# Kernel tuning notes

Hardware: AMD Instinct MI355X
Metric: run time of the kernel (lower is better)

The kernel has to match this reference:

```python
import jax, jax.numpy as jnp
import numpy as np

B, T, D, H = 4, 2048, 1024, 16
HD = D // H  # head_size = 64
EPS = 1e-5


def layernorm(x, g, b):
    mu = jnp.mean(x, axis=-1, keepdims=True)
    var = jnp.var(x, axis=-1, keepdims=True)
    return (x - mu) * jax.lax.rsqrt(var + EPS) * g + b


def setup_inputs() -> dict:
    key = jax.random.key(0)
    ks = jax.random.split(key, 8)
    s = 0.02
    return {
        "x": jax.random.normal(ks[0], (B, T, D), jnp.float32),
        "Wq": jax.random.normal(ks[1], (D, D), jnp.float32) * s,
        "Wk": jax.random.normal(ks[2], (D, D), jnp.float32) * s,
        "Wv": jax.random.normal(ks[3], (D, D), jnp.float32) * s,
        "Wo": jax.random.normal(ks[4], (D, D), jnp.float32) * s,
        "bo": jnp.zeros((D,), jnp.float32),
        "W1": jax.random.normal(ks[5], (D, 4 * D), jnp.float32) * s,
        "b1": jnp.zeros((4 * D,), jnp.float32),
        "W2": jax.random.normal(ks[6], (4 * D, D), jnp.float32) * s,
        "b2": jnp.zeros((D,), jnp.float32),
        "ln1_g": jnp.ones((D,), jnp.float32),
        "ln1_b": jnp.zeros((D,), jnp.float32),
        "ln2_g": jnp.ones((D,), jnp.float32),
        "ln2_b": jnp.zeros((D,), jnp.float32),
    }


def reference(x, Wq, Wk, Wv, Wo, bo, W1, b1, W2, b2, ln1_g, ln1_b, ln2_g, ln2_b):
    # --- multi-head causal self-attention (pre-LN), dropout off (eval) ---
    h = layernorm(x, ln1_g, ln1_b)
    q = jnp.einsum('btd,de->bte', h, Wq).reshape(B, T, H, HD)
    k = jnp.einsum('btd,de->bte', h, Wk).reshape(B, T, H, HD)
    v = jnp.einsum('btd,de->bte', h, Wv).reshape(B, T, H, HD)
    scores = jnp.einsum('bqhd,bkhd->bhqk', q, k) * (HD ** -0.5)
    causal = jnp.tril(jnp.ones((T, T), bool))
    scores = jnp.where(causal, scores, -jnp.inf)
    attn = jax.nn.softmax(scores, axis=-1)
    out = jnp.einsum('bhqk,bkhd->bqhd', attn, v).reshape(B, T, D)
    out = jnp.einsum('btd,de->bte', out, Wo) + bo
    x = x + out
    # --- feed-forward: Linear -> ReLU -> Linear -> ReLU (as in source) ---
    h2 = layernorm(x, ln2_g, ln2_b)
    ff = jax.nn.relu(jnp.einsum('btd,df->btf', h2, W1) + b1)
    ff = jax.nn.relu(jnp.einsum('btf,fd->btd', ff, W2) + b2)
    return x + ff
```

## Files before the change

### kernel.cpp

```cpp
#include <hip/hip_runtime.h>
#include <cstdint>
#include <cstddef>

typedef unsigned short u16;
typedef __attribute__((ext_vector_type(8))) short bf16x8;
typedef __attribute__((ext_vector_type(4))) float f32x4;
typedef __attribute__((address_space(1))) const unsigned int gu32;
typedef __attribute__((address_space(3))) unsigned int lu32;

#define QSCALE 0.1803368801111204f

__device__ __forceinline__ u16 f2bf(float f) {
  uint32_t u = __float_as_uint(f);
  u += 0x7fffu + ((u >> 16) & 1u);
  return (u16)(u >> 16);
}

__device__ __forceinline__ void xcd_swz(int& bn, int& bm) {
  int gx = (int)gridDim.x;
  int n = gx * (int)gridDim.y;
  int lid = (int)blockIdx.x + gx * (int)blockIdx.y;
  int nid = (lid & 7) * (n >> 3) + (lid >> 3);
  bn = nid % gx;
  bm = nid / gx;
}

__global__ __launch_bounds__(256) void transpose_w(const float* __restrict__ W,
                                                   u16* __restrict__ WT,
                                                   int K, int N) {
  __shared__ float t[32][33];
  int n0 = blockIdx.x * 32, k0 = blockIdx.y * 32;
  for (int i = threadIdx.y; i < 32; i += 8)
    t[i][threadIdx.x] = W[(size_t)(k0 + i) * N + n0 + threadIdx.x];
  __syncthreads();
  for (int i = threadIdx.y; i < 32; i += 8)
    WT[(size_t)(n0 + i) * K + k0 + threadIdx.x] = f2bf(t[threadIdx.x][i]);
}

__global__ __launch_bounds__(256) void ln_kernel(const float* __restrict__ x,
                                                 const float* __restrict__ g,
                                                 const float* __restrict__ b,
                                                 u16* __restrict__ out) {
  int row = blockIdx.x;
  const float4 v = *(const float4*)(x + (size_t)row * 1024 + threadIdx.x * 4);
  float s = v.x + v.y + v.z + v.w;
  float ss = v.x * v.x + v.y * v.y + v.z * v.z + v.w * v.w;
#pragma unroll
  for (int d = 1; d < 64; d <<= 1) { s += __shfl_xor(s, d); ss += __shfl_xor(ss, d); }
  __shared__ float rs_[4], rss_[4];
  int wv = threadIdx.x >> 6;
  if ((threadIdx.x & 63) == 0) { rs_[wv] = s; rss_[wv] = ss; }
  __syncthreads();
  s = rs_[0] + rs_[1] + rs_[2] + rs_[3];
  ss = rss_[0] + rss_[1] + rss_[2] + rss_[3];
  float mu = s * (1.f / 1024.f);
  float var = ss * (1.f / 1024.f) - mu * mu;
  float rstd = rsqrtf(var + 1e-5f);
  float4 gv = *(const float4*)(g + threadIdx.x * 4);
  float4 bv = *(const float4*)(b + threadIdx.x * 4);
  uint32_t lo = (uint32_t)f2bf((v.x - mu) * rstd * gv.x + bv.x) |
                ((uint32_t)f2bf((v.y - mu) * rstd * gv.y + bv.y) << 16);
  uint32_t hi = (uint32_t)f2bf((v.z - mu) * rstd * gv.z + bv.z) |
                ((uint32_t)f2bf((v.w - mu) * rstd * gv.w + bv.w) << 16);
  uint2 o; o.x = lo; o.y = hi;
  *(uint2*)(out + (size_t)row * 1024 + threadIdx.x * 4) = o;
}

#define G128A(is)                                                             \
  __builtin_amdgcn_global_load_lds(                                           \
      (gu32*)((const char*)(A + (size_t)(bm * 128 + (is) * 32 + srow) * K +   \
                            (size_t)kt * 64) + ssw),                          \
      (lu32*)&lds[(is) * 2048 + wid * 512], 16, 0, 0)
#define G128B(is)                                                             \
  __builtin_amdgcn_global_load_lds(                                           \
      (gu32*)((const char*)(BT + (size_t)(bn * 128 + (is) * 32 + srow) * K +  \
                            (size_t)kt * 64) + ssw),                          \
      (lu32*)&lds[8192 + (is) * 2048 + wid * 512], 16, 0, 0)

template <int MODE>
__global__ __launch_bounds__(256, 4) void g128(
    const u16* __restrict__ A, const u16* __restrict__ BT,
    int M, int N, int K,
    const float* __restrict__ bias, const float* __restrict__ resid,
    float* __restrict__ outf,
    u16* __restrict__ ob0, u16* __restrict__ ob1, u16* __restrict__ ob2) {
  __shared__ __align__(16) u16 lds[16384];
  const int tid = threadIdx.x, lane = tid & 63, wid = tid >> 6;
  const int wr = wid >> 1, wc = wid & 1;
  int bn, bm;
  xcd_swz(bn, bm);
  const int l15 = lane & 15, lhi = lane >> 4;
  const int srow = tid >> 3;
  const int ssw = ((tid & 7) * 16) ^ ((srow & 7) << 4);
  const int swz = (l15 & 7) << 4;
  const int cb0 = (lhi * 16) ^ swz;
  const int cb1 = (64 + lhi * 16) ^ swz;
  const char* Ab = (const char*)lds;
  const char* Bb = (const char*)lds + 16384;

  f32x4 acc[4][4];
#pragma unroll
  for (int i = 0; i < 4; ++i)
#pragma unroll
    for (int j = 0; j < 4; ++j) acc[i][j] = (f32x4){0.f, 0.f, 0.f, 0.f};

  const int NT = K >> 6;

  for (int kt = 0; kt < NT; ++kt) {
    __syncthreads();
    G128A(0); G128A(1); G128A(2); G128A(3);
    G128B(0); G128B(1); G128B(2); G128B(3);
    __syncthreads();
#pragma unroll
    for (int ks = 0; ks < 2; ++ks) {
      const int cb = ks ? cb1 : cb0;
      bf16x8 af[4], bf[4];
#pragma unroll
      for (int mi = 0; mi < 4; ++mi)
        af[mi] = *(const bf16x8*)(Ab + (wr * 64 + mi * 16 + l15) * 128 + cb);
#pragma unroll
      for (int ni = 0; ni < 4; ++ni)
        bf[ni] = *(const bf16x8*)(Bb + (wc * 64 + ni * 16 + l15) * 128 + cb);
#pragma unroll
      for (int mi = 0; mi < 4; ++mi)
#pragma unroll
        for (int ni = 0; ni < 4; ++ni)
          acc[mi][ni] = __builtin_amdgcn_mfma_f32_16x16x32_bf16(af[mi], bf[ni], acc[mi][ni], 0, 0, 0);
    }
  }

  char* ep = (char*)lds;
  if (MODE == 0 && bn >= 16) {
#pragma unroll
    for (int h = 0; h < 2; ++h) {
      __syncthreads();
      if (wc == h) {
#pragma unroll
        for (int mi = 0; mi < 4; ++mi)
#pragma unroll
          for (int ni = 0; ni < 4; ++ni) {
            uint32_t lo, hi;
            asm("v_cvt_pk_bf16_f32 %0, %1, %2"
                : "=v"(lo) : "v"(acc[mi][ni][0]), "v"(acc[mi][ni][1]));
            asm("v_cvt_pk_bf16_f32 %0, %1, %2"
                : "=v"(hi) : "v"(acc[mi][ni][2]), "v"(acc[mi][ni][3]));
            uint2 pk; pk.x = lo; pk.y = hi;
            int c_local = ni * 16 + l15;
            int rb = wr * 64 + mi * 16 + lhi * 4;
            *(uint2*)(ep + c_local * 264 + rb * 2) = pk;
          }
      }
      __syncthreads();
#pragma unroll
      for (int it = 0; it < 4; ++it) {
        int idx = it * 256 + tid;
        int c = idx >> 4, tc = idx & 15;
        uint4 d4 = *(const uint4*)(ep + c * 264 + tc * 16);
        int cm = bn * 128 + h * 64 + c - 2048, hh = cm >> 6, dd = cm & 63;
        size_t bh = (size_t)((bm >> 4) * 16 + hh);
        int t0 = (bm & 15) * 128;
        *(uint4*)&ob2[(bh * 64 + dd) * 2048 + t0 + tc * 8] = d4;
      }
    }
  } else if (MODE == 0 || MODE == 2) {
    const float sc = (MODE == 0 && bn < 8) ? QSCALE : 1.f;
#pragma unroll
    for (int h = 0; h < 2; ++h) {
      __syncthreads();
      if (wr == h) {
#pragma unroll
        for (int mi = 0; mi < 4; ++mi)
#pragma unroll
          for (int ni = 0; ni < 4; ++ni) {
            int c_local = wc * 64 + ni * 16 + l15;
            int rb = mi * 16 + lhi * 4;
            float bv = (MODE == 2) ? bias[bn * 128 + c_local] : 0.f;
#pragma unroll
            for (int r = 0; r < 4; ++r) {
              float v = acc[mi][ni][r];
              v = (MODE == 2) ? fmaxf(v + bv, 0.f) : v * sc;
              *(u16*)(ep + (rb + r) * 272 + c_local * 2) = f2bf(v);
            }
          }
      }
      __syncthreads();
#pragma unroll
      for (int it = 0; it < 4; ++it) {
        int idx = it * 256 + tid;
        int row = idx >> 4, cc = idx & 15;
        uint4 d4 = *(const uint4*)(ep + row * 272 + cc * 16);
        size_t rg = (size_t)(bm * 128 + h * 64 + row);
        int colg = bn * 128 + cc * 8;
        if (MODE == 2) {
          *(uint4*)&ob0[rg * (size_t)N + colg] = d4;
        } else if (colg < 1024) {
          *(uint4*)&ob0[rg * 1024 + colg] = d4;
        } else {
          *(uint4*)&ob1[rg * 1024 + colg - 1024] = d4;
        }
      }
    }
  } else {
    float* epf = (float*)lds;
#pragma unroll
    for (int q = 0; q < 4; ++q) {
      __syncthreads();
      if (wr == (q >> 1)) {
#pragma unroll
        for (int mh = 0; mh < 2; ++mh) {
          int mi = (q & 1) * 2 + mh;
#pragma unroll
          for (int ni = 0; ni < 4; ++ni) {
            int c_local = wc * 64 + ni * 16 + l15;
            int rl = mh * 16 + lhi * 4;
#pragma unroll
            for (int r = 0; r < 4; ++r)
              epf[(rl + r) * 132 + c_local] = acc[mi][ni][r];
          }
        }
      }
      __syncthreads();
#pragma unroll
      for (int it = 0; it < 4; ++it) {
        int idx = it * 256 + tid;
        int row = idx >> 5, cc = idx & 31;
        float4 v = *(const float4*)&epf[row * 132 + cc * 4];
        int colg = bn * 128 + cc * 4;
        size_t rg = (size_t)(bm * 128 + q * 32 + row);
        float4 bv = *(const float4*)&bias[colg];
        float4 rv = *(const float4*)&resid[rg * (size_t)N + colg];
        float4 o4;
        if (MODE == 1) {
          o4.x = v.x + bv.x + rv.x; o4.y = v.y + bv.y + rv.y;
          o4.z = v.z + bv.z + rv.z; o4.w = v.w + bv.w + rv.w;
        } else {
          o4.x = fmaxf(v.x + bv.x, 0.f) + rv.x;
          o4.y = fmaxf(v.y + bv.y, 0.f) + rv.y;
          o4.z = fmaxf(v.z + bv.z, 0.f) + rv.z;
          o4.w = fmaxf(v.w + bv.w, 0.f) + rv.w;
        }
        *(float4*)&outf[rg * (size_t)N + colg] = o4;
      }
    }
  }
}

__global__ __launch_bounds__(512) void attn_kernel(
    const u16* __restrict__ Qb, const u16* __restrict__ Kb,
    const u16* __restrict__ VTb, u16* __restrict__ O) {
  const int lid = (int)blockIdx.x + 8 * (int)blockIdx.y;
  const int p = (lid >> 3) & 7;
  const int bh = ((lid >> 6) << 3) | (lid & 7);
  const int b = bh >> 4, h = bh & 15;
  const u16* Q = Qb + (size_t)b * 2048 * 1024 + h * 64;
  const u16* Kn = Kb + (size_t)b * 2048 * 1024 + h * 64;
  const u16* VT = VTb + (size_t)bh * 64 * 2048;
  const int tid = threadIdx.x, lane = tid & 63, wv = tid >> 6;
  const int l15 = lane & 15, lhi = lane >> 4;
  const int srow = tid >> 3;
  const int scol16 = (tid & 7) * 16;
  const int sw = scol16 ^ ((srow & 7) << 4);
  const int rswz = (l15 & 7) << 4;
  const int cb0 = (lhi * 16) ^ rswz;
  const int cb1 = (64 + lhi * 16) ^ rswz;

  __shared__ __align__(16) u16 KV[2][2][4096];
  __shared__ u16 Ps[8][16 * 72];

  bf16x8 onesf;
#pragma unroll
  for (int i = 0; i < 8; ++i) onesf[i] = (short)0x3F80;

#define STAGEKV(slot, kt)                                                     \
  do {                                                                        \
    __builtin_amdgcn_global_load_lds(                                         \
        (gu32*)((const char*)(Kn + (size_t)((kt)*64 + srow) * 1024) + sw),    \
        (lu32*)&KV[slot][0][wv * 512], 16, 0, 0);                             \
    __builtin_amdgcn_global_load_lds(                                         \
        (gu32*)((const char*)(VT + (size_t)srow * 2048 + (kt)*64) + sw),      \
        (lu32*)&KV[slot][1][wv * 512], 16, 0, 0);                             \
  } while (0)

#pragma unroll
  for (int pass = 0; pass < 2; ++pass) {
    const int chunk = pass ? p : (15 - p);
    const int qbase = chunk * 128 + wv * 16;
    const int nkt = 2 * chunk + 2;

    bf16x8 qf[2];
#pragma unroll
    for (int ks = 0; ks < 2; ++ks)
      qf[ks] = *(const bf16x8*)&Q[(size_t)(qbase + l15) * 1024 + ks * 32 + lhi * 8];

    f32x4 o[4];
#pragma unroll
    for (int f = 0; f < 4; ++f) o[f] = (f32x4){0.f, 0.f, 0.f, 0.f};
    f32x4 lacc = (f32x4){0.f, 0.f, 0.f, 0.f};

    __syncthreads();
    STAGEKV(0, 0);

    for (int kt = 0; kt < nkt; ++kt) {
      const int cs = kt & 1;
      asm volatile("s_waitcnt vmcnt(0)" ::: "memory");
      __syncthreads();
      if (kt + 1 < nkt) STAGEKV(cs ^ 1, kt + 1);

      if (kt * 64 <= qbase + 15) {
        const char* Kbase = (const char*)&KV[cs][0][0];
        const char* Vbase = (const char*)&KV[cs][1][0];

        f32x4 s[4];
#pragma unroll
        for (int jt = 0; jt < 4; ++jt) s[jt] = (f32x4){0.f, 0.f, 0.f, 0.f};
        __builtin_amdgcn_s_setprio(1);
#pragma unroll
        for (int ks = 0; ks < 2; ++ks) {
          const int cbyte = ks ? cb1 : cb0;
#pragma unroll
          for (int jt = 0; jt < 4; ++jt) {
            bf16x8 kf = *(const bf16x8*)(Kbase + (jt * 16 + l15) * 128 + cbyte);
            s[jt] = __builtin_amdgcn_mfma_f32_16x16x32_bf16(kf, qf[ks], s[jt], 0, 0, 0);
          }
        }
        __builtin_amdgcn_s_setprio(0);

        if (kt * 64 + 63 > qbase) {
          int qg = qbase + l15;
#pragma unroll
          for (int jt = 0; jt < 4; ++jt)
#pragma unroll
            for (int r = 0; r < 4; ++r) {
              int kg = kt * 64 + jt * 16 + lhi * 4 + r;
              if (kg > qg) s[jt][r] = -1e30f;
            }
        }

#pragma unroll
        for (int jt = 0; jt < 4; ++jt)
#pragma unroll
          for (int r = 0; r < 4; ++r) s[jt][r] = exp2f(s[jt][r]);

#pragma unroll
        for (int jt = 0; jt < 4; ++jt) {
          uint32_t lo, hi;
          asm("v_cvt_pk_bf16_f32 %0, %1, %2"
              : "=v"(lo) : "v"(s[jt][0]), "v"(s[jt][1]));
          asm("v_cvt_pk_bf16_f32 %0, %1, %2"
              : "=v"(hi) : "v"(s[jt][2]), "v"(s[jt][3]));
          uint2 pk; pk.x = lo; pk.y = hi;
          *(uint2*)&Ps[wv][l15 * 72 + jt * 16 + lhi * 4] = pk;
        }
        __builtin_amdgcn_s_setprio(1);
#pragma unroll
        for (int ks = 0; ks < 2; ++ks) {
          const int cbyte = ks ? cb1 : cb0;
          bf16x8 pf = *(const bf16x8*)&Ps[wv][l15 * 72 + ks * 32 + lhi * 8];
          lacc = __builtin_amdgcn_mfma_f32_16x16x32_bf16(pf, onesf, lacc, 0, 0, 0);
#pragma unroll
          for (int f = 0; f < 4; ++f) {
            bf16x8 vfr = *(const bf16x8*)(Vbase + (f * 16 + l15) * 128 + cbyte);
            o[f] = __builtin_amdgcn_mfma_f32_16x16x32_bf16(pf, vfr, o[f], 0, 0, 0);
          }
        }
        __builtin_amdgcn_s_setprio(0);
      }
    }

#pragma unroll
    for (int r = 0; r < 4; ++r) {
      float inv = 1.f / lacc[r];
      int t = qbase + lhi * 4 + r;
#pragma unroll
      for (int f = 0; f < 4; ++f)
        O[((size_t)(b * 2048 + t)) * 1024 + h * 64 + f * 16 + l15] = f2bf(o[f][r] * inv);
    }
  }
#undef STAGEKV
}

extern "C" void kernel_launch(void* const* d_in, const int* in_sizes, int n_in,
                              void* d_out, int out_size, void* d_ws, size_t ws_size,
                              hipStream_t stream) {
  const float* x   = (const float*)d_in[0];
  const float* Wq  = (const float*)d_in[1];
  const float* Wk  = (const float*)d_in[2];
  const float* Wv  = (const float*)d_in[3];
  const float* Wo  = (const float*)d_in[4];
  const float* bo  = (const float*)d_in[5];
  const float* W1  = (const float*)d_in[6];
  const float* b1  = (const float*)d_in[7];
  const float* W2  = (const float*)d_in[8];
  const float* b2  = (const float*)d_in[9];
  const float* g1  = (const float*)d_in[10];
  const float* be1 = (const float*)d_in[11];
  const float* g2  = (const float*)d_in[12];
  const float* be2 = (const float*)d_in[13];

  char* p = (char*)d_ws;
  auto alloc = [&](size_t bytes) {
    char* r = p;
    p += (bytes + 255) & ~(size_t)255;
    return r;
  };
  u16* WqkvT = (u16*)alloc(3072ull * 1024 * 2);
  u16* WoT   = (u16*)alloc(1024ull * 1024 * 2);
  u16* W1T   = (u16*)alloc(4096ull * 1024 * 2);
  u16* W2T   = (u16*)alloc(1024ull * 4096 * 2);
  u16* hln   = (u16*)alloc(8192ull * 1024 * 2);
  u16* Qbuf  = (u16*)alloc(8192ull * 1024 * 2);
  u16* Kbuf  = (u16*)alloc(8192ull * 1024 * 2);
  u16* VTbuf = (u16*)alloc(8192ull * 1024 * 2);
  float* x2  = (float*)alloc(8192ull * 1024 * 4);
  u16* ff1   = (u16*)alloc(8192ull * 4096 * 2);
  u16* Oattn = hln;
  u16* h2    = Qbuf;
  if ((size_t)(p - (char*)d_ws) > ws_size) return;

  dim3 tb(32, 8);
  transpose_w<<<dim3(32, 32), tb, 0, stream>>>(Wq, WqkvT, 1024, 1024);
  transpose_w<<<dim3(32, 32), tb, 0, stream>>>(Wk, WqkvT + 1024 * 1024, 1024, 1024);
  transpose_w<<<dim3(32, 32), tb, 0, stream>>>(Wv, WqkvT + 2048 * 1024, 1024, 1024);
  transpose_w<<<dim3(32, 32), tb, 0, stream>>>(Wo, WoT, 1024, 1024);
  transpose_w<<<dim3(128, 32), tb, 0, stream>>>(W1, W1T, 1024, 4096);
  transpose_w<<<dim3(32, 128), tb, 0, stream>>>(W2, W2T, 4096, 1024);

  ln_kernel<<<8192, 256, 0, stream>>>(x, g1, be1, hln);

  g128<0><<<dim3(24, 64), 256, 0, stream>>>(hln, WqkvT, 8192, 3072, 1024,
                                            nullptr, nullptr, nullptr,
                                            Qbuf, Kbuf, VTbuf);

  attn_kernel<<<dim3(8, 64), 512, 0, stream>>>(Qbuf, Kbuf, VTbuf, Oattn);

  g128<1><<<dim3(8, 64), 256, 0, stream>>>(Oattn, WoT, 8192, 1024, 1024,
                                           bo, x, x2, nullptr, nullptr, nullptr);

  ln_kernel<<<8192, 256, 0, stream>>>(x2, g2, be2, h2);

  g128<2><<<dim3(32, 64), 256, 0, stream>>>(h2, W1T, 8192, 4096, 1024,
                                            b1, nullptr, nullptr, ff1, nullptr, nullptr);

  g128<3><<<dim3(8, 64), 256, 0, stream>>>(ff1, W2T, 8192, 1024, 4096,
                                           b2, x2, (float*)d_out, nullptr, nullptr, nullptr);
}
```

Baseline: 375.5 us.

## Use 128x64 GEMM tiles for N=1024 projections and smaller attention blocks

Adds a 128x64-tile GEMM kernel for the Wo and W2 projections (N=1024), which doubles the grid from 512 to 1024 blocks so the CUs are better filled. The attention kernel moves from 512 to 256 threads with 64-row query chunks, doubling its grid. It also swizzles the P scratch buffer in LDS to avoid bank conflicts, and merges four weight-transpose launches into one. Smaller tiles cut per-block data reuse and the new GEMM has no double buffering, so it may lose efficiency on the K=4096 FF2 GEMM.

```diff
diff --git a/kernel.cpp b/kernel.cpp
--- a/kernel.cpp
+++ b/kernel.cpp
@@ -35,6 +35,24 @@
   __syncthreads();
   for (int i = threadIdx.y; i < 32; i += 8)
     WT[(size_t)(n0 + i) * K + k0 + threadIdx.x] = f2bf(t[threadIdx.x][i]);
+}
+
+__global__ __launch_bounds__(256) void transpose_w4(
+    const float* __restrict__ W0, const float* __restrict__ W1,
+    const float* __restrict__ W2, const float* __restrict__ W3,
+    u16* __restrict__ D0, u16* __restrict__ D1,
+    u16* __restrict__ D2, u16* __restrict__ D3) {
+  __shared__ float t[32][33];
+  const float* W = (blockIdx.z == 0) ? W0 : (blockIdx.z == 1) ? W1
+                   : (blockIdx.z == 2) ? W2 : W3;
+  u16* D = (blockIdx.z == 0) ? D0 : (blockIdx.z == 1) ? D1
+           : (blockIdx.z == 2) ? D2 : D3;
+  int n0 = blockIdx.x * 32, k0 = blockIdx.y * 32;
+  for (int i = threadIdx.y; i < 32; i += 8)
+    t[i][threadIdx.x] = W[(size_t)(k0 + i) * 1024 + n0 + threadIdx.x];
+  __syncthreads();
+  for (int i = threadIdx.y; i < 32; i += 8)
+    D[(size_t)(n0 + i) * 1024 + k0 + threadIdx.x] = f2bf(t[threadIdx.x][i]);
 }
 
 __global__ __launch_bounds__(256) void ln_kernel(const float* __restrict__ x,
@@ -81,8 +99,7 @@
 __global__ __launch_bounds__(256, 4) void g128(
     const u16* __restrict__ A, const u16* __restrict__ BT,
     int M, int N, int K,
-    const float* __restrict__ bias, const float* __restrict__ resid,
-    float* __restrict__ outf,
+    const float* __restrict__ bias,
     u16* __restrict__ ob0, u16* __restrict__ ob1, u16* __restrict__ ob2) {
   __shared__ __align__(16) u16 lds[16384];
   const int tid = threadIdx.x, lane = tid & 63, wid = tid >> 6;
@@ -162,7 +179,7 @@
         *(uint4*)&ob2[(bh * 64 + dd) * 2048 + t0 + tc * 8] = d4;
       }
     }
-  } else if (MODE == 0 || MODE == 2) {
+  } else {
     const float sc = (MODE == 0 && bn < 8) ? QSCALE : 1.f;
 #pragma unroll
     for (int h = 0; h < 2; ++h) {
@@ -200,57 +217,118 @@
         }
       }
     }
-  } else {
-    float* epf = (float*)lds;
-#pragma unroll
-    for (int q = 0; q < 4; ++q) {
-      __syncthreads();
-      if (wr == (q >> 1)) {
-#pragma unroll
-        for (int mh = 0; mh < 2; ++mh) {
-          int mi = (q & 1) * 2 + mh;
-#pragma unroll
-          for (int ni = 0; ni < 4; ++ni) {
-            int c_local = wc * 64 + ni * 16 + l15;
-            int rl = mh * 16 + lhi * 4;
-#pragma unroll
-            for (int r = 0; r < 4; ++r)
-              epf[(rl + r) * 132 + c_local] = acc[mi][ni][r];
-          }
+  }
+}
+
+#define G64A(is)                                                              \
+  __builtin_amdgcn_global_load_lds(                                           \
+      (gu32*)((const char*)(A + (size_t)(bm * 128 + (is) * 32 + srow) * K +   \
+                            (size_t)kt * 64) + ssw),                          \
+      (lu32*)&lds[(is) * 2048 + wid * 512], 16, 0, 0)
+#define G64B(is)                                                              \
+  __builtin_amdgcn_global_load_lds(                                           \
+      (gu32*)((const char*)(BT + (size_t)(bn * 64 + (is) * 32 + srow) * K +   \
+                            (size_t)kt * 64) + ssw),                          \
+      (lu32*)&lds[8192 + (is) * 2048 + wid * 512], 16, 0, 0)
+
+template <int MODE>
+__global__ __launch_bounds__(256, 4) void g64n(
+    const u16* __restrict__ A, const u16* __restrict__ BT,
+    int M, int N, int K,
+    const float* __restrict__ bias, const float* __restrict__ resid,
+    float* __restrict__ outf) {
+  __shared__ __align__(16) u16 lds[12288];
+  const int tid = threadIdx.x, lane = tid & 63, wid = tid >> 6;
+  const int wr = wid >> 1, wc = wid & 1;
+  int bn, bm;
+  xcd_swz(bn, bm);
+  const int l15 = lane & 15, lhi = lane >> 4;
+  const int srow = tid >> 3;
+  const int ssw = ((tid & 7) * 16) ^ ((srow & 7) << 4);
+  const int swz = (l15 & 7) << 4;
+  const int cb0 = (lhi * 16) ^ swz;
+  const int cb1 = (64 + lhi * 16) ^ swz;
+  const char* Ab = (const char*)lds;
+  const char* Bb = (const char*)lds + 16384;
+
+  f32x4 acc[4][2];
+#pragma unroll
+  for (int i = 0; i < 4; ++i)
+#pragma unroll
+    for (int j = 0; j < 2; ++j) acc[i][j] = (f32x4){0.f, 0.f, 0.f, 0.f};
+
+  const int NT = K >> 6;
+
+  for (int kt = 0; kt < NT; ++kt) {
+    __syncthreads();
+    G64A(0); G64A(1); G64A(2); G64A(3);
+    G64B(0); G64B(1);
+    __syncthreads();
+#pragma unroll
+    for (int ks = 0; ks < 2; ++ks) {
+      const int cb = ks ? cb1 : cb0;
+      bf16x8 af[4], bf[2];
+#pragma unroll
+      for (int mi = 0; mi < 4; ++mi)
+        af[mi] = *(const bf16x8*)(Ab + (wr * 64 + mi * 16 + l15) * 128 + cb);
+#pragma unroll
+      for (int ni = 0; ni < 2; ++ni)
+        bf[ni] = *(const bf16x8*)(Bb + (wc * 32 + ni * 16 + l15) * 128 + cb);
+#pragma unroll
+      for (int mi = 0; mi < 4; ++mi)
+#pragma unroll
+        for (int ni = 0; ni < 2; ++ni)
+          acc[mi][ni] = __builtin_amdgcn_mfma_f32_16x16x32_bf16(af[mi], bf[ni], acc[mi][ni], 0, 0, 0);
+    }
+  }
+
+  float* epf = (float*)lds;
+#pragma unroll
+  for (int h = 0; h < 2; ++h) {
+    __syncthreads();
+    if (wr == h) {
+#pragma unroll
+      for (int mi = 0; mi < 4; ++mi)
+#pragma unroll
+        for (int ni = 0; ni < 2; ++ni) {
+          int c_local = wc * 32 + ni * 16 + l15;
+          int rl = mi * 16 + lhi * 4;
+#pragma unroll
+          for (int r = 0; r < 4; ++r)
+            epf[(rl + r) * 68 + c_local] = acc[mi][ni][r];
         }
+    }
+    __syncthreads();
+#pragma unroll
+    for (int it = 0; it < 4; ++it) {
+      int idx = it * 256 + tid;
+      int row = idx >> 4, cc = idx & 15;
+      float4 v = *(const float4*)&epf[row * 68 + cc * 4];
+      int colg = bn * 64 + cc * 4;
+      size_t rg = (size_t)(bm * 128 + h * 64 + row);
+      float4 bv = *(const float4*)&bias[colg];
+      float4 rv = *(const float4*)&resid[rg * (size_t)N + colg];
+      float4 o4;
+      if (MODE == 1) {
+        o4.x = v.x + bv.x + rv.x; o4.y = v.y + bv.y + rv.y;
+        o4.z = v.z + bv.z + rv.z; o4.w = v.w + bv.w + rv.w;
+      } else {
+        o4.x = fmaxf(v.x + bv.x, 0.f) + rv.x;
+        o4.y = fmaxf(v.y + bv.y, 0.f) + rv.y;
+        o4.z = fmaxf(v.z + bv.z, 0.f) + rv.z;
+        o4.w = fmaxf(v.w + bv.w, 0.f) + rv.w;
       }
-      __syncthreads();
-#pragma unroll
-      for (int it = 0; it < 4; ++it) {
-        int idx = it * 256 + tid;
-        int row = idx >> 5, cc = idx & 31;
-        float4 v = *(const float4*)&epf[row * 132 + cc * 4];
-        int colg = bn * 128 + cc * 4;
-        size_t rg = (size_t)(bm * 128 + q * 32 + row);
-        float4 bv = *(const float4*)&bias[colg];
-        float4 rv = *(const float4*)&resid[rg * (size_t)N + colg];
-        float4 o4;
-        if (MODE == 1) {
-          o4.x = v.x + bv.x + rv.x; o4.y = v.y + bv.y + rv.y;
-          o4.z = v.z + bv.z + rv.z; o4.w = v.w + bv.w + rv.w;
-        } else {
-          o4.x = fmaxf(v.x + bv.x, 0.f) + rv.x;
-          o4.y = fmaxf(v.y + bv.y, 0.f) + rv.y;
-          o4.z = fmaxf(v.z + bv.z, 0.f) + rv.z;
-          o4.w = fmaxf(v.w + bv.w, 0.f) + rv.w;
-        }
-        *(float4*)&outf[rg * (size_t)N + colg] = o4;
-      }
+      *(float4*)&outf[rg * (size_t)N + colg] = o4;
     }
   }
 }
 
-__global__ __launch_bounds__(512) void attn_kernel(
+__global__ __launch_bounds__(256) void attn_kernel(
     const u16* __restrict__ Qb, const u16* __restrict__ Kb,
     const u16* __restrict__ VTb, u16* __restrict__ O) {
-  const int lid = (int)blockIdx.x + 8 * (int)blockIdx.y;
-  const int p = (lid >> 3) & 7;
-  const int bh = ((lid >> 6) << 3) | (lid & 7);
+  const int lid = (int)blockIdx.x + 16 * (int)blockIdx.y;
+  const int p = (lid >> 3) & 15;
+  const int bh = ((lid >> 7) << 3) | (lid & 7);
   const int b = bh >> 4, h = bh & 15;
   const u16* Q = Qb + (size_t)b * 2048 * 1024 + h * 64;
   const u16* Kn = Kb + (size_t)b * 2048 * 1024 + h * 64;
@@ -263,9 +341,12 @@
   const int rswz = (l15 & 7) << 4;
   const int cb0 = (lhi * 16) ^ rswz;
   const int cb1 = (64 + lhi * 16) ^ rswz;
+  const int psw = (l15 & 7) << 4;
 
   __shared__ __align__(16) u16 KV[2][2][4096];
-  __shared__ u16 Ps[8][16 * 72];
+  __shared__ __align__(16) u16 Ps[4][1024];
+
+  char* Pw = (char*)&Ps[wv][0];
 
   bf16x8 onesf;
 #pragma unroll
@@ -277,15 +358,21 @@
         (gu32*)((const char*)(Kn + (size_t)((kt)*64 + srow) * 1024) + sw),    \
         (lu32*)&KV[slot][0][wv * 512], 16, 0, 0);                             \
     __builtin_amdgcn_global_load_lds(                                         \
+        (gu32*)((const char*)(Kn + (size_t)((kt)*64 + 32 + srow) * 1024) + sw), \
+        (lu32*)&KV[slot][0][2048 + wv * 512], 16, 0, 0);                      \
+    __builtin_amdgcn_global_load_lds(                                         \
         (gu32*)((const char*)(VT + (size_t)srow * 2048 + (kt)*64) + sw),      \
         (lu32*)&KV[slot][1][wv * 512], 16, 0, 0);                             \
+    __builtin_amdgcn_global_load_lds(                                         \
+        (gu32*)((const char*)(VT + (size_t)(32 + srow) * 2048 + (kt)*64) + sw), \
+        (lu32*)&KV[slot][1][2048 + wv * 512], 16, 0, 0);                      \
   } while (0)
 
 #pragma unroll
   for (int pass = 0; pass < 2; ++pass) {
-    const int chunk = pass ? p : (15 - p);
-    const int qbase = chunk * 128 + wv * 16;
-    const int nkt = 2 * chunk + 2;
+    const int chunk = pass ? p : (31 - p);
+    const int qbase = chunk * 64 + wv * 16;
+    const int nkt = chunk + 1;
 
     bf16x8 qf[2];
 #pragma unroll
@@ -349,13 +436,13 @@
           asm("v_cvt_pk_bf16_f32 %0, %1, %2"
               : "=v"(hi) : "v"(s[jt][2]), "v"(s[jt][3]));
           uint2 pk; pk.x = lo; pk.y = hi;
-          *(uint2*)&Ps[wv][l15 * 72 + jt * 16 + lhi * 4] = pk;
+          *(uint2*)(Pw + ((l15 * 128 + jt * 32 + lhi * 8) ^ psw)) = pk;
         }
         __builtin_amdgcn_s_setprio(1);
 #pragma unroll
         for (int ks = 0; ks < 2; ++ks) {
           const int cbyte = ks ? cb1 : cb0;
-          bf16x8 pf = *(const bf16x8*)&Ps[wv][l15 * 72 + ks * 32 + lhi * 8];
+          bf16x8 pf = *(const bf16x8*)(Pw + ((l15 * 128 + ks * 64 + lhi * 16) ^ psw));
           lacc = __builtin_amdgcn_mfma_f32_16x16x32_bf16(pf, onesf, lacc, 0, 0, 0);
 #pragma unroll
           for (int f = 0; f < 4; ++f) {
@@ -418,29 +505,26 @@
   if ((size_t)(p - (char*)d_ws) > ws_size) return;
 
   dim3 tb(32, 8);
-  transpose_w<<<dim3(32, 32), tb, 0, stream>>>(Wq, WqkvT, 1024, 1024);
-  transpose_w<<<dim3(32, 32), tb, 0, stream>>>(Wk, WqkvT + 1024 * 1024, 1024, 1024);
-  transpose_w<<<dim3(32, 32), tb, 0, stream>>>(Wv, WqkvT + 2048 * 1024, 1024, 1024);
-  transpose_w<<<dim3(32, 32), tb, 0, stream>>>(Wo, WoT, 1024, 1024);
+  transpose_w4<<<dim3(32, 32, 4), tb, 0, stream>>>(
+      Wq, Wk, Wv, Wo, WqkvT, WqkvT + 1024 * 1024, WqkvT + 2048 * 1024, WoT);
   transpose_w<<<dim3(128, 32), tb, 0, stream>>>(W1, W1T, 1024, 4096);
   transpose_w<<<dim3(32, 128), tb, 0, stream>>>(W2, W2T, 4096, 1024);
 
   ln_kernel<<<8192, 256, 0, stream>>>(x, g1, be1, hln);
 
   g128<0><<<dim3(24, 64), 256, 0, stream>>>(hln, WqkvT, 8192, 3072, 1024,
-                                            nullptr, nullptr, nullptr,
-                                            Qbuf, Kbuf, VTbuf);
-
-  attn_kernel<<<dim3(8, 64), 512, 0, stream>>>(Qbuf, Kbuf, VTbuf, Oattn);
-
-  g128<1><<<dim3(8, 64), 256, 0, stream>>>(Oattn, WoT, 8192, 1024, 1024,
-                                           bo, x, x2, nullptr, nullptr, nullptr);
+                                            nullptr, Qbuf, Kbuf, VTbuf);
+
+  attn_kernel<<<dim3(16, 64), 256, 0, stream>>>(Qbuf, Kbuf, VTbuf, Oattn);
+
+  g64n<1><<<dim3(16, 64), 256, 0, stream>>>(Oattn, WoT, 8192, 1024, 1024,
+                                            bo, x, x2);
 
   ln_kernel<<<8192, 256, 0, stream>>>(x2, g2, be2, h2);
 
   g128<2><<<dim3(32, 64), 256, 0, stream>>>(h2, W1T, 8192, 4096, 1024,
-                                            b1, nullptr, nullptr, ff1, nullptr, nullptr);
-
-  g128<3><<<dim3(8, 64), 256, 0, stream>>>(ff1, W2T, 8192, 1024, 4096,
-                                           b2, x2, (float*)d_out, nullptr, nullptr, nullptr);
-}
+                                            b1, ff1, nullptr, nullptr);
+
+  g64n<3><<<dim3(16, 64), 256, 0, stream>>>(ff1, W2T, 8192, 1024, 4096,
+                                            b2, x2, (float*)d_out);
+}
```

After: 383.9 us. 2.2% more time.
